# Optimization experiments

Measured on AMD Instinct MI355X. Metric: run time of the kernel, lower is better.

Reference implementation:

```python
import jax, jax.numpy as jnp
import numpy as np
from jax.scipy.special import logsumexp

TAU = 0.05
N_ITERS = 10
LR = 0.5
BETA1 = 0.9
BETA2 = 0.999
EPS_ADAM = 1e-8
BATCH, N, M = 16, 1024, 1024


def setup_inputs() -> dict:
    key = jax.random.key(0)
    k1, k2, k3 = jax.random.split(key, 3)
    log_alpha = jax.random.normal(k1, (BATCH, N, M), dtype=jnp.float32)
    # valid log-marginals (rows of log_alpha's transport plan must sum to exp(log_a))
    log_a = jax.nn.log_softmax(jax.random.normal(k2, (BATCH, N), dtype=jnp.float32), axis=-1)
    log_b = jax.nn.log_softmax(jax.random.normal(k3, (BATCH, M), dtype=jnp.float32), axis=-1)
    return {"log_alpha": log_alpha, "log_a": log_a, "log_b": log_b}


def _sinkhorn_adam(log_alpha, log_a, log_b):
    kernel = log_alpha / TAU  # [B, N, M]
    b, n, m = log_alpha.shape
    u = jnp.zeros((b, n), dtype=log_alpha.dtype)
    v = jnp.zeros((b, m), dtype=log_alpha.dtype)
    m_u = jnp.zeros_like(u)
    v_u = jnp.zeros_like(u)
    m_v = jnp.zeros_like(v)
    v_v = jnp.zeros_like(v)

    def step(carry, iter_idx):
        u, v, m_u, v_u, m_v, v_v = carry
        t = (iter_idx + 1).astype(log_alpha.dtype)
        bc1 = 1.0 - jnp.power(jnp.asarray(BETA1, log_alpha.dtype), t)
        bc2 = 1.0 - jnp.power(jnp.asarray(BETA2, log_alpha.dtype), t)

        # u update (Adam on the fixed-point residual)
        u_target = log_a - logsumexp(kernel + v[:, None, :], axis=-1)
        g_u = u_target - u
        m_u = BETA1 * m_u + (1.0 - BETA1) * g_u
        v_u = BETA2 * v_u + (1.0 - BETA2) * (g_u * g_u)
        u_next = u + LR * (m_u / bc1) / (jnp.sqrt(v_u / bc2) + EPS_ADAM)

        # v update using the fresh u
        v_target = log_b - logsumexp(kernel + u_next[:, :, None], axis=-2)
        g_v = v_target - v
        m_v = BETA1 * m_v + (1.0 - BETA1) * g_v
        v_v = BETA2 * v_v + (1.0 - BETA2) * (g_v * g_v)
        v_next = v + LR * (m_v / bc1) / (jnp.sqrt(v_v / bc2) + EPS_ADAM)

        return (u_next, v_next, m_u, v_u, m_v, v_v), None

    (u, v, m_u, v_u, m_v, v_v), _ = jax.lax.scan(
        step, (u, v, m_u, v_u, m_v, v_v), jnp.arange(N_ITERS))
    # transport plan
    return jnp.exp(kernel + u[:, :, None] + v[:, None, :])


def reference(log_alpha, log_a, log_b):
    return _sinkhorn_adam(log_alpha, log_a, log_b)
```

## Files before the change

kernel.cpp:

```cpp
#include <hip/hip_runtime.h>
#include <cmath>

#define BB 16
#define NN 1024
#define MM 1024

#define RPB   32
#define RREG  16
#define RLDS  (RPB - RREG)
#define NGRP  (NN / RPB)
#define NBLK  (BB * NGRP)

#define RPB8  8
#define NSLAB (NN / RPB8)

static constexpr float INV_TAU = 20.0f;
static constexpr float LR   = 0.5f;
static constexpr float B1f  = 0.9f;
static constexpr float B2f  = 0.999f;
static constexpr float EPSA = 1e-8f;
static constexpr float EXP_CAP = 88.0f;

#define OFF_U    0
#define OFF_V    16384
#define OFF_MU   32768
#define OFF_VU   49152
#define OFF_MV   65536
#define OFF_VV   81920
#define OFF_CNT  98304
#define OFF_PART 102400

#define CNT_ROOT 2048
#define CNT_FLAG 2080

__device__ __forceinline__ void st_sc1_f2(float2* p, float mx, float sy) {
    union { float2 f; unsigned long long u; } cv; cv.f = make_float2(mx, sy);
    __hip_atomic_store((unsigned long long*)p, cv.u, __ATOMIC_RELAXED, __HIP_MEMORY_SCOPE_AGENT);
}
__device__ __forceinline__ float2 ld_sc1_f2(const float2* p) {
    union { float2 f; unsigned long long u; } cv;
    cv.u = __hip_atomic_load((unsigned long long*)p, __ATOMIC_RELAXED, __HIP_MEMORY_SCOPE_AGENT);
    return cv.f;
}
__device__ __forceinline__ void st_sc1_f(float* p, float v) {
    union { float f; unsigned u; } cv; cv.f = v;
    __hip_atomic_store((unsigned*)p, cv.u, __ATOMIC_RELAXED, __HIP_MEMORY_SCOPE_AGENT);
}
__device__ __forceinline__ float4 ld_sc1_f4(const float* p) {
    const float2 a = ld_sc1_f2((const float2*)p);
    const float2 b = ld_sc1_f2((const float2*)(p + 2));
    return make_float4(a.x, a.y, b.x, b.y);
}

__device__ __forceinline__ void gbar(int* cb, int bid, int& ep) {
    __syncthreads();
    ++ep;
    if (threadIdx.x == 0) {
        asm volatile("s_waitcnt vmcnt(0)" ::: "memory");
        const int old = __hip_atomic_fetch_add(cb + ((bid >> 3) << 5), 1,
                          __ATOMIC_RELAXED, __HIP_MEMORY_SCOPE_AGENT);
        if (old == ep * 8 - 1) {
            const int ro = __hip_atomic_fetch_add(cb + CNT_ROOT, 1,
                             __ATOMIC_RELAXED, __HIP_MEMORY_SCOPE_AGENT);
            if (ro == ep * 64 - 1)
                __hip_atomic_store(cb + CNT_FLAG, ep,
                                   __ATOMIC_RELAXED, __HIP_MEMORY_SCOPE_AGENT);
        }
        while (__hip_atomic_load(cb + CNT_FLAG, __ATOMIC_RELAXED,
                                 __HIP_MEMORY_SCOPE_AGENT) < ep)
            __builtin_amdgcn_s_sleep(2);
    }
    __syncthreads();
}

__global__ __launch_bounds__(256)
__attribute__((amdgpu_waves_per_eu(2, 2)))
void sinkhorn_persistent(
    const float* __restrict__ la, const float* __restrict__ log_a,
    const float* __restrict__ log_b, float* __restrict__ ws,
    float2* __restrict__ part, float* __restrict__ out)
{
    const int bid  = blockIdx.x;
    const int b    = bid >> 5;
    const int g    = bid & 31;
    const int row0 = g * RPB;
    const int tid  = threadIdx.x;
    const int wave = tid >> 6;
    const int lane = tid & 63;

    __shared__ float  klds[RLDS][MM];
    __shared__ float  redm[4 * RPB];
    __shared__ float  reds[4 * RPB];
    __shared__ float  fin[RPB];
    __shared__ float  su[RPB];
    __shared__ float2 red2[8][32];

    int* cb = (int*)ws + OFF_CNT;
    int ep = 0;

    const float* Kb = la + ((size_t)b * NN + row0) * MM + 4 * tid;
    float kr[RREG][4];
#pragma unroll
    for (int r = 0; r < RREG; ++r) {
        const float4 k4 = *(const float4*)(Kb + (size_t)r * MM);
        kr[r][0] = k4.x * INV_TAU; kr[r][1] = k4.y * INV_TAU;
        kr[r][2] = k4.z * INV_TAU; kr[r][3] = k4.w * INV_TAU;
    }
#pragma unroll
    for (int r = 0; r < RLDS; ++r) {
        float4 k4 = *(const float4*)(Kb + (size_t)(RREG + r) * MM);
        k4.x *= INV_TAU; k4.y *= INV_TAU; k4.z *= INV_TAU; k4.w *= INV_TAU;
        *(float4*)(&klds[r][4 * tid]) = k4;
    }
    __syncthreads();

    float pb1 = 1.0f, pb2 = 1.0f;
    for (int t = 0; t < 10; ++t) {
        pb1 *= B1f; pb2 *= B2f;
        const float bc1 = 1.0f - pb1, bc2 = 1.0f - pb2;

        const float4 v4 = ld_sc1_f4(ws + OFF_V + b * MM + 4 * tid);
#pragma unroll
        for (int r = 0; r < RREG; ++r) {
            float m = fmaxf(fmaxf(kr[r][0] + v4.x, kr[r][1] + v4.y),
                            fmaxf(kr[r][2] + v4.z, kr[r][3] + v4.w));
#pragma unroll
            for (int off = 32; off; off >>= 1) m = fmaxf(m, __shfl_xor(m, off, 64));
            if (lane == 0) redm[wave * RPB + r] = m;
        }
#pragma unroll
        for (int r = 0; r < RLDS; ++r) {
            const float4 k4 = *(const float4*)(&klds[r][4 * tid]);
            float m = fmaxf(fmaxf(k4.x + v4.x, k4.y + v4.y),
                            fmaxf(k4.z + v4.z, k4.w + v4.w));
#pragma unroll
            for (int off = 32; off; off >>= 1) m = fmaxf(m, __shfl_xor(m, off, 64));
            if (lane == 0) redm[wave * RPB + RREG + r] = m;
        }
        __syncthreads();
        if (tid < RPB)
            fin[tid] = fmaxf(fmaxf(redm[tid], redm[RPB + tid]),
                             fmaxf(redm[2 * RPB + tid], redm[3 * RPB + tid]));
        __syncthreads();

#pragma unroll
        for (int r = 0; r < RREG; ++r) {
            const float Mr = fin[r];
            float s = __expf(kr[r][0] + v4.x - Mr) + __expf(kr[r][1] + v4.y - Mr)
                    + __expf(kr[r][2] + v4.z - Mr) + __expf(kr[r][3] + v4.w - Mr);
#pragma unroll
            for (int off = 32; off; off >>= 1) s += __shfl_xor(s, off, 64);
            if (lane == 0) reds[wave * RPB + r] = s;
        }
#pragma unroll
        for (int r = 0; r < RLDS; ++r) {
            const float4 k4 = *(const float4*)(&klds[r][4 * tid]);
            const float Mr = fin[RREG + r];
            float s = __expf(k4.x + v4.x - Mr) + __expf(k4.y + v4.y - Mr)
                    + __expf(k4.z + v4.z - Mr) + __expf(k4.w + v4.w - Mr);
#pragma unroll
            for (int off = 32; off; off >>= 1) s += __shfl_xor(s, off, 64);
            if (lane == 0) reds[wave * RPB + RREG + r] = s;
        }
        __syncthreads();
        if (tid < RPB) {
            const int r  = tid;
            const int gi = b * NN + row0 + r;
            const float S   = reds[r] + reds[RPB + r] + reds[2 * RPB + r] + reds[3 * RPB + r];
            const float lse = fin[r] + __logf(S);
            const float uo  = ws[OFF_U + gi];
            const float gu  = (log_a[gi] - lse) - uo;
            const float m_  = B1f * ws[OFF_MU + gi] + (1.f - B1f) * gu;
            const float v_  = B2f * ws[OFF_VU + gi] + (1.f - B2f) * gu * gu;
            ws[OFF_MU + gi] = m_;
            ws[OFF_VU + gi] = v_;
            const float un  = uo + LR * (m_ / bc1) / (sqrtf(v_ / bc2) + EPSA);
            ws[OFF_U + gi]  = un;
            su[r] = un;
        }
        __syncthreads();

        {
            float cm[4];
#pragma unroll
            for (int j = 0; j < 4; ++j) cm[j] = kr[0][j] + su[0];
#pragma unroll
            for (int r = 1; r < RREG; ++r) {
                const float sr = su[r];
                cm[0] = fmaxf(cm[0], kr[r][0] + sr);
                cm[1] = fmaxf(cm[1], kr[r][1] + sr);
                cm[2] = fmaxf(cm[2], kr[r][2] + sr);
                cm[3] = fmaxf(cm[3], kr[r][3] + sr);
            }
#pragma unroll
            for (int r = 0; r < RLDS; ++r) {
                const float4 k4 = *(const float4*)(&klds[r][4 * tid]);
                const float sr = su[RREG + r];
                cm[0] = fmaxf(cm[0], k4.x + sr);
                cm[1] = fmaxf(cm[1], k4.y + sr);
                cm[2] = fmaxf(cm[2], k4.z + sr);
                cm[3] = fmaxf(cm[3], k4.w + sr);
            }
            float cs[4] = {0.f, 0.f, 0.f, 0.f};
#pragma unroll
            for (int r = 0; r < RREG; ++r) {
                const float sr = su[r];
                cs[0] += __expf(kr[r][0] + sr - cm[0]);
                cs[1] += __expf(kr[r][1] + sr - cm[1]);
                cs[2] += __expf(kr[r][2] + sr - cm[2]);
                cs[3] += __expf(kr[r][3] + sr - cm[3]);
            }
#pragma unroll
            for (int r = 0; r < RLDS; ++r) {
                const float4 k4 = *(const float4*)(&klds[r][4 * tid]);
                const float sr = su[RREG + r];
                cs[0] += __expf(k4.x + sr - cm[0]);
                cs[1] += __expf(k4.y + sr - cm[1]);
                cs[2] += __expf(k4.z + sr - cm[2]);
                cs[3] += __expf(k4.w + sr - cm[3]);
            }
            float2* p = part + ((size_t)b * NGRP + g) * MM + 4 * tid;
            st_sc1_f2(p + 0, cm[0], cs[0]);
            st_sc1_f2(p + 1, cm[1], cs[1]);
            st_sc1_f2(p + 2, cm[2], cs[2]);
            st_sc1_f2(p + 3, cm[3], cs[3]);
        }
        gbar(cb, bid, ep);

        {
            const int c32 = tid & 31;
            const int q   = tid >> 5;
            const float2* pp = part + ((size_t)b * NGRP + q * 4) * MM + (g * 32 + c32);
            float Mc = -3.0e38f, Sc = 0.f;
#pragma unroll
            for (int s5 = 0; s5 < 4; ++s5) {
                const float2 pr = ld_sc1_f2(pp + (size_t)s5 * MM);
                const float mn = fmaxf(Mc, pr.x);
                Sc = Sc * __expf(Mc - mn) + pr.y * __expf(pr.x - mn);
                Mc = mn;
            }
            red2[q][c32] = make_float2(Mc, Sc);
            __syncthreads();
            if (tid < 32) {
                float M = -3.0e38f, S = 0.f;
#pragma unroll
                for (int q2 = 0; q2 < 8; ++q2) {
                    const float2 pr = red2[q2][tid];
                    const float mn = fmaxf(M, pr.x);
                    S = S * __expf(M - mn) + pr.y * __expf(pr.x - mn);
                    M = mn;
                }
                const int i     = b * MM + g * 32 + tid;
                const float lse = M + __logf(S);
                const float vo  = ws[OFF_V + i];
                const float gv  = (log_b[i] - lse) - vo;
                const float m_  = B1f * ws[OFF_MV + i] + (1.f - B1f) * gv;
                const float v_  = B2f * ws[OFF_VV + i] + (1.f - B2f) * gv * gv;
                ws[OFF_MV + i] = m_;
                ws[OFF_VV + i] = v_;
                st_sc1_f(ws + OFF_V + i, vo + LR * (m_ / bc1) / (sqrtf(v_ / bc2) + EPSA));
            }
        }
        gbar(cb, bid, ep);
    }

    const float4 vf = ld_sc1_f4(ws + OFF_V + b * MM + 4 * tid);
    float* ob = out + ((size_t)b * NN + row0) * MM + 4 * tid;
#pragma unroll
    for (int r = 0; r < RREG; ++r) {
        const float uu = su[r];
        float4 o;
        o.x = __expf(fminf(kr[r][0] + uu + vf.x, EXP_CAP));
        o.y = __expf(fminf(kr[r][1] + uu + vf.y, EXP_CAP));
        o.z = __expf(fminf(kr[r][2] + uu + vf.z, EXP_CAP));
        o.w = __expf(fminf(kr[r][3] + uu + vf.w, EXP_CAP));
        *(float4*)(ob + (size_t)r * MM) = o;
    }
#pragma unroll
    for (int r = 0; r < RLDS; ++r) {
        const float4 k4 = *(const float4*)(&klds[r][4 * tid]);
        const float uu = su[RREG + r];
        float4 o;
        o.x = __expf(fminf(k4.x + uu + vf.x, EXP_CAP));
        o.y = __expf(fminf(k4.y + uu + vf.y, EXP_CAP));
        o.z = __expf(fminf(k4.z + uu + vf.z, EXP_CAP));
        o.w = __expf(fminf(k4.w + uu + vf.w, EXP_CAP));
        *(float4*)(ob + (size_t)(RREG + r) * MM) = o;
    }
}

__global__ __launch_bounds__(256, 4) void iter_fused(
    const float* __restrict__ la, const float* __restrict__ log_a,
    float* __restrict__ ws, float2* __restrict__ part,
    float bc1, float bc2)
{
    const int slab = blockIdx.x;
    const int b    = blockIdx.y;
    const int row0 = slab * RPB8;
    const int tid  = threadIdx.x;
    const int wave = tid >> 6;
    const int lane = tid & 63;
    __shared__ float redm[4 * RPB8];
    __shared__ float reds[4 * RPB8];
    __shared__ float fin[RPB8];
    __shared__ float su[RPB8];

    const float* Kb = la + ((size_t)b * NN + row0) * MM + 4 * tid;
    float kr[RPB8][4];
#pragma unroll
    for (int r = 0; r < RPB8; ++r) {
        const float4 k4 = *(const float4*)(Kb + (size_t)r * MM);
        kr[r][0] = k4.x * INV_TAU; kr[r][1] = k4.y * INV_TAU;
        kr[r][2] = k4.z * INV_TAU; kr[r][3] = k4.w * INV_TAU;
    }
    const float4 v4 = *(const float4*)(ws + OFF_V + b * MM + 4 * tid);
    const float vj[4] = {v4.x, v4.y, v4.z, v4.w};

    float pm[RPB8];
#pragma unroll
    for (int r = 0; r < RPB8; ++r)
        pm[r] = fmaxf(fmaxf(kr[r][0] + vj[0], kr[r][1] + vj[1]),
                      fmaxf(kr[r][2] + vj[2], kr[r][3] + vj[3]));
#pragma unroll
    for (int off = 32; off; off >>= 1)
#pragma unroll
        for (int r = 0; r < RPB8; ++r)
            pm[r] = fmaxf(pm[r], __shfl_xor(pm[r], off, 64));
    if (lane == 0)
#pragma unroll
        for (int r = 0; r < RPB8; ++r) redm[wave * RPB8 + r] = pm[r];
    __syncthreads();
    if (tid < RPB8)
        fin[tid] = fmaxf(fmaxf(redm[tid], redm[RPB8 + tid]),
                         fmaxf(redm[2 * RPB8 + tid], redm[3 * RPB8 + tid]));
    __syncthreads();
    float Mr[RPB8];
#pragma unroll
    for (int r = 0; r < RPB8; ++r) Mr[r] = fin[r];

    float ps[RPB8];
#pragma unroll
    for (int r = 0; r < RPB8; ++r)
        ps[r] = __expf(kr[r][0] + vj[0] - Mr[r]) + __expf(kr[r][1] + vj[1] - Mr[r])
              + __expf(kr[r][2] + vj[2] - Mr[r]) + __expf(kr[r][3] + vj[3] - Mr[r]);
#pragma unroll
    for (int off = 32; off; off >>= 1)
#pragma unroll
        for (int r = 0; r < RPB8; ++r)
            ps[r] += __shfl_xor(ps[r], off, 64);
    if (lane == 0)
#pragma unroll
        for (int r = 0; r < RPB8; ++r) reds[wave * RPB8 + r] = ps[r];
    __syncthreads();
    if (tid < RPB8) {
        const int r  = tid;
        const int gi = b * NN + row0 + r;
        const float S   = reds[r] + reds[RPB8 + r] + reds[2 * RPB8 + r] + reds[3 * RPB8 + r];
        const float lse = Mr[r] + __logf(S);
        const float uo  = ws[OFF_U + gi];
        const float gu  = (log_a[gi] - lse) - uo;
        const float m_  = B1f * ws[OFF_MU + gi] + (1.f - B1f) * gu;
        const float v_  = B2f * ws[OFF_VU + gi] + (1.f - B2f) * gu * gu;
        ws[OFF_MU + gi] = m_;
        ws[OFF_VU + gi] = v_;
        const float un  = uo + LR * (m_ / bc1) / (sqrtf(v_ / bc2) + EPSA);
        ws[OFF_U + gi]  = un;
        su[r] = un;
    }
    __syncthreads();
    float uu[RPB8];
#pragma unroll
    for (int r = 0; r < RPB8; ++r) uu[r] = su[r];

    float2 out4[4];
#pragma unroll
    for (int j = 0; j < 4; ++j) {
        float m = kr[0][j] + uu[0];
#pragma unroll
        for (int r = 1; r < RPB8; ++r) m = fmaxf(m, kr[r][j] + uu[r]);
        float s = 0.f;
#pragma unroll
        for (int r = 0; r < RPB8; ++r) s += __expf(kr[r][j] + uu[r] - m);
        out4[j] = make_float2(m, s);
    }
    float2* p = part + ((size_t)b * NSLAB + slab) * MM + 4 * tid;
    p[0] = out4[0]; p[1] = out4[1]; p[2] = out4[2]; p[3] = out4[3];
}

__global__ __launch_bounds__(256, 8) void combine_legacy(
    const float* __restrict__ log_b, float* __restrict__ ws,
    const float2* __restrict__ part, float bc1, float bc2)
{
    const int b   = blockIdx.x >> 4;
    const int mg  = blockIdx.x & 15;
    const int tid = threadIdx.x;
    const int c   = tid & 63;
    const int q   = tid >> 6;
    const int m   = mg * 64 + c;
    __shared__ float2 red[4][64];

    const float2* p = part + ((size_t)b * NSLAB + q * 32) * MM + m;
    float M = -3.0e38f, S = 0.f;
#pragma unroll 8
    for (int s = 0; s < 32; ++s) {
        const float2 pr = p[(size_t)s * MM];
        const float mn = fmaxf(M, pr.x);
        S = S * __expf(M - mn) + pr.y * __expf(pr.x - mn);
        M = mn;
    }
    red[q][c] = make_float2(M, S);
    __syncthreads();
    if (q == 0) {
        const float2 a = red[0][c], bb = red[1][c], cc = red[2][c], d = red[3][c];
        const float Mt = fmaxf(fmaxf(a.x, bb.x), fmaxf(cc.x, d.x));
        const float St = a.y * __expf(a.x - Mt) + bb.y * __expf(bb.x - Mt)
                       + cc.y * __expf(cc.x - Mt) + d.y * __expf(d.x - Mt);
        const int i = b * MM + m;
        const float lse = Mt + __logf(St);
        const float vo  = ws[OFF_V + i];
        const float gv  = (log_b[i] - lse) - vo;
        const float m_  = B1f * ws[OFF_MV + i] + (1.f - B1f) * gv;
        const float v_  = B2f * ws[OFF_VV + i] + (1.f - B2f) * gv * gv;
        ws[OFF_MV + i] = m_;
        ws[OFF_VV + i] = v_;
        ws[OFF_V + i]  = vo + LR * (m_ / bc1) / (sqrtf(v_ / bc2) + EPSA);
    }
}

__global__ void finalize_legacy(const float* __restrict__ la, const float* __restrict__ ws,
                                float* __restrict__ out)
{
    const size_t i4 = (size_t)blockIdx.x * 256 + threadIdx.x;
    const size_t e  = i4 * 4;
    const int row = (int)(e >> 10);
    const int b   = row >> 10;
    const int m   = (int)(e & 1023);
    const float uu = ws[OFF_U + row];
    const float4 k4 = ((const float4*)la)[i4];
    const float4 v4 = *(const float4*)(ws + OFF_V + b * MM + m);
    float4 o;
    o.x = __expf(fminf(k4.x * INV_TAU + uu + v4.x, EXP_CAP));
    o.y = __expf(fminf(k4.y * INV_TAU + uu + v4.y, EXP_CAP));
    o.z = __expf(fminf(k4.z * INV_TAU + uu + v4.z, EXP_CAP));
    o.w = __expf(fminf(k4.w * INV_TAU + uu + v4.w, EXP_CAP));
    ((float4*)out)[i4] = o;
}

extern "C" void kernel_launch(void* const* d_in, const int* in_sizes, int n_in,
                              void* d_out, int out_size, void* d_ws, size_t ws_size,
                              hipStream_t stream) {
    const float* la    = (const float*)d_in[0];
    const float* log_a = (const float*)d_in[1];
    const float* log_b = (const float*)d_in[2];
    float*  out  = (float*)d_out;
    float*  ws   = (float*)d_ws;
    float2* part = (float2*)(ws + OFF_PART);

    hipMemsetAsync(d_ws, 0, OFF_PART * sizeof(float), stream);

    void* args[] = {(void*)&la, (void*)&log_a, (void*)&log_b,
                    (void*)&ws, (void*)&part, (void*)&out};
    hipError_t err = hipLaunchCooperativeKernel(
        (const void*)sinkhorn_persistent, dim3(NBLK), dim3(256), args, 0, stream);

    if (err != hipSuccess) {
        for (int t = 1; t <= 10; ++t) {
            const float bc1 = 1.0f - powf(B1f, (float)t);
            const float bc2 = 1.0f - powf(B2f, (float)t);
            iter_fused<<<dim3(NSLAB, BB), 256, 0, stream>>>(la, log_a, ws, part, bc1, bc2);
            combine_legacy<<<BB * MM / 256, 256, 0, stream>>>(log_b, ws, part, bc1, bc2);
        }
        finalize_legacy<<<16384, 256, 0, stream>>>(la, ws, out);
    }
}
```

Baseline: 418.5 us.

## Replace grid-wide atomic barrier with per-batch flag barrier

Replaces the two-level atomic-counter barrier across all 512 blocks with a barrier scoped to each batch's 32 blocks. Each block stores its epoch to its own slot, block 0 of the batch polls all 32 slots with one wavefront and then publishes a per-batch release flag that the other blocks spin on. This removes atomic read-modify-write contention and the global dependency between batches, since batches only exchange data inside their own group. The risks are that dropping the explicit vmcnt wait and using relaxed stores may weaken ordering of the partial-result writes, and that the polling adds more memory traffic.

After: 386.1 us. -7.7%, faster.

```diff
diff --git a/kernel.cpp b/kernel.cpp
--- a/kernel.cpp
+++ b/kernel.cpp
@@ -30,8 +30,7 @@
 #define OFF_CNT  98304
 #define OFF_PART 102400
 
-#define CNT_ROOT 2048
-#define CNT_FLAG 2080
+#define FLAG_BASE 1024
 
 __device__ __forceinline__ void st_sc1_f2(float2* p, float mx, float sy) {
     union { float2 f; unsigned long long u; } cv; cv.f = make_float2(mx, sy);
@@ -52,23 +51,29 @@
     return make_float4(a.x, a.y, b.x, b.y);
 }
 
-__device__ __forceinline__ void gbar(int* cb, int bid, int& ep) {
+__device__ __forceinline__ void gbar(int* cb, int b, int g, int& ep) {
     __syncthreads();
     ++ep;
-    if (threadIdx.x == 0) {
-        asm volatile("s_waitcnt vmcnt(0)" ::: "memory");
-        const int old = __hip_atomic_fetch_add(cb + ((bid >> 3) << 5), 1,
-                          __ATOMIC_RELAXED, __HIP_MEMORY_SCOPE_AGENT);
-        if (old == ep * 8 - 1) {
-            const int ro = __hip_atomic_fetch_add(cb + CNT_ROOT, 1,
-                             __ATOMIC_RELAXED, __HIP_MEMORY_SCOPE_AGENT);
-            if (ro == ep * 64 - 1)
-                __hip_atomic_store(cb + CNT_FLAG, ep,
+    const int tid = threadIdx.x;
+    if (tid == 0)
+        __hip_atomic_store(cb + b * 64 + g, ep,
+                           __ATOMIC_RELAXED, __HIP_MEMORY_SCOPE_AGENT);
+    if (g == 0) {
+        if (tid < 64) {
+            for (;;) {
+                const int v = __hip_atomic_load(cb + b * 64 + (tid & 31),
+                                __ATOMIC_RELAXED, __HIP_MEMORY_SCOPE_AGENT);
+                if (__all(v >= ep)) break;
+                __builtin_amdgcn_s_sleep(1);
+            }
+            if (tid == 0)
+                __hip_atomic_store(cb + FLAG_BASE + b * 32, ep,
                                    __ATOMIC_RELAXED, __HIP_MEMORY_SCOPE_AGENT);
         }
-        while (__hip_atomic_load(cb + CNT_FLAG, __ATOMIC_RELAXED,
-                                 __HIP_MEMORY_SCOPE_AGENT) < ep)
-            __builtin_amdgcn_s_sleep(2);
+    } else if (tid == 0) {
+        while (__hip_atomic_load(cb + FLAG_BASE + b * 32,
+                 __ATOMIC_RELAXED, __HIP_MEMORY_SCOPE_AGENT) < ep)
+            __builtin_amdgcn_s_sleep(1);
     }
     __syncthreads();
 }
@@ -225,7 +230,7 @@
             st_sc1_f2(p + 2, cm[2], cs[2]);
             st_sc1_f2(p + 3, cm[3], cs[3]);
         }
-        gbar(cb, bid, ep);
+        gbar(cb, b, g, ep);
 
         {
             const int c32 = tid & 31;
@@ -261,7 +266,7 @@
                 st_sc1_f(ws + OFF_V + i, vo + LR * (m_ / bc1) / (sqrtf(v_ / bc2) + EPSA));
             }
         }
-        gbar(cb, bid, ep);
+        gbar(cb, b, g, ep);
     }
 
     const float4 vf = ld_sc1_f4(ws + OFF_V + b * MM + 4 * tid);
```
